# Kernel tuning notes

Hardware: AMD Instinct MI355X
Metric: run time of the kernel (lower is better)

## Reference

```python
import jax, jax.numpy as jnp
import numpy as np
from jax import lax

B, W, L, K = 256, 4096, 16, 8  # batch, nodes/level, levels, fan-in


def setup_inputs() -> dict:
    key = jax.random.key(0)
    ks = jax.random.split(key, 7)
    s = 1.0 / np.sqrt(K)  # torch nn.Linear default init scale
    observed_bits = jnp.round(jax.random.uniform(ks[0], (B, W))).astype(jnp.float32)
    prior_w = jax.random.uniform(ks[1], (W,), minval=-1.0, maxval=1.0)  # PriorNode Linear(1,1) weight
    prior_b = jax.random.uniform(ks[2], (W,), minval=-1.0, maxval=1.0)
    weights = jax.random.uniform(ks[3], (L - 1, W, K), minval=-s, maxval=s)  # per-node Linear(K,1)
    biases = jax.random.uniform(ks[4], (L - 1, W), minval=-s, maxval=s)
    # parents sorted DESCENDING per node: heap pops higher rv first, so inputs are
    # concatenated in descending parent-rv order in the original traversal.
    parents = -jnp.sort(-jax.random.randint(ks[5], (L - 1, W, K), 0, W), axis=-1)
    inv_mask = jax.random.randint(ks[6], (L - 1, W), 0, 2).astype(bool)  # True -> InvNode
    return {"observed_bits": observed_bits, "prior_w": prior_w, "prior_b": prior_b,
            "weights": weights, "biases": biases, "parents": parents, "inv_mask": inv_mask}


def reference(observed_bits, prior_w, prior_b, weights, biases, parents, inv_mask):
    # Observed level: PriorNode with num_parents=1 -> relu(w*bit + b), per node.  (B, W)
    h = jax.nn.relu(observed_bits * prior_w[None, :] + prior_b[None, :])

    def step(h, lvl):
        w, b, p, inv = lvl  # (W,K), (W,), (W,K) int, (W,) bool
        x = h[:, p]                                   # gather parent outputs -> (B, W, K)
        x = jnp.where(inv[:, None], 1.0 - x, x)       # InvNode applies fc(1 - x)
        h2 = jax.nn.relu(jnp.einsum('bnk,nk->bn', x, w) + b)  # per-node Linear(K,1)+ReLU
        return h2, None

    h, _ = lax.scan(step, h, (weights, biases, parents, inv_mask))
    return h  # (B, num_input_bits) == pred.squeeze() of the original
```

## Files before the change

kernel.cpp:

```cpp
#include <hip/hip_runtime.h>
#include <hip/hip_fp16.h>

#define WN 4096
#define BN 256
#define KN 8
#define NLVL 15
#define NTHR 1024
#define NPT (WN / NTHR)

__global__ __launch_bounds__(256) void prep_kernel(
    const float* __restrict__ wts, const float* __restrict__ bia,
    const int* __restrict__ par,   const int* __restrict__ inv,
    uint4* __restrict__ Wh, uint4* __restrict__ Pp, float* __restrict__ Bz) {
  __shared__ unsigned cnt[4][32];
  const int t    = threadIdx.x;
  const int wv   = t >> 6;
  const int lane = t & 63;
  const int idx  = blockIdx.x * 256 + t;
  unsigned* c = cnt[wv];

  const int4   pA = *(const int4*)(par + (size_t)idx * KN);
  const int4   pB = *(const int4*)(par + (size_t)idx * KN + 4);
  const float4 wA = *(const float4*)(wts + (size_t)idx * KN);
  const float4 wB = *(const float4*)(wts + (size_t)idx * KN + 4);
  const bool   iv = inv[idx] != 0;
  const float  sw = ((wA.x + wA.y) + (wA.z + wA.w)) + ((wB.x + wB.y) + (wB.z + wB.w));
  const float  s  = iv ? -1.0f : 1.0f;
  const int   p0 = pA.x, p1 = pA.y, p2 = pA.z, p3 = pA.w;
  const int   p4 = pB.x, p5 = pB.y, p6 = pB.z, p7 = pB.w;
  const float w0 = wA.x * s, w1 = wA.y * s, w2 = wA.z * s, w3 = wA.w * s;
  const float w4 = wB.x * s, w5 = wB.y * s, w6 = wB.z * s, w7 = wB.w * s;

  unsigned mask = 0xffu;
  unsigned op[KN];
  float    ow[KN];

#pragma unroll
  for (int k = 0; k < KN; ++k) {
    __syncthreads();
    if (lane < 32) c[lane] = 0;
    __syncthreads();
    unsigned bestj = 0, bestv = 0xffffffffu;
#define SCAN(J, PJ) if (mask & (1u << (J))) { unsigned v = c[(PJ) & 31]; if (v < bestv) { bestv = v; bestj = (J); } }
    SCAN(0, p0) SCAN(1, p1) SCAN(2, p2) SCAN(3, p3)
    SCAN(4, p4) SCAN(5, p5) SCAN(6, p6) SCAN(7, p7)
#undef SCAN
    const unsigned pj =
        (bestj == 0) ? (unsigned)p0 : (bestj == 1) ? (unsigned)p1 :
        (bestj == 2) ? (unsigned)p2 : (bestj == 3) ? (unsigned)p3 :
        (bestj == 4) ? (unsigned)p4 : (bestj == 5) ? (unsigned)p5 :
        (bestj == 6) ? (unsigned)p6 : (unsigned)p7;
    const float wj =
        (bestj == 0) ? w0 : (bestj == 1) ? w1 :
        (bestj == 2) ? w2 : (bestj == 3) ? w3 :
        (bestj == 4) ? w4 : (bestj == 5) ? w5 :
        (bestj == 6) ? w6 : w7;
    atomicAdd(&c[pj & 31], 1u);
    op[k] = pj;
    ow[k] = wj;
    mask &= ~(1u << bestj);
  }

  Pp[idx] = make_uint4(op[0] | (op[1] << 16), op[2] | (op[3] << 16),
                       op[4] | (op[5] << 16), op[6] | (op[7] << 16));
  uint4 wq;
  wq.x = (unsigned)__half_as_ushort(__float2half(ow[0])) |
         ((unsigned)__half_as_ushort(__float2half(ow[1])) << 16);
  wq.y = (unsigned)__half_as_ushort(__float2half(ow[2])) |
         ((unsigned)__half_as_ushort(__float2half(ow[3])) << 16);
  wq.z = (unsigned)__half_as_ushort(__float2half(ow[4])) |
         ((unsigned)__half_as_ushort(__float2half(ow[5])) << 16);
  wq.w = (unsigned)__half_as_ushort(__float2half(ow[6])) |
         ((unsigned)__half_as_ushort(__float2half(ow[7])) << 16);
  Wh[idx] = wq;
  Bz[idx] = iv ? bia[idx] + sw : bia[idx];
}

__global__ __launch_bounds__(NTHR) void fused_lds_kernel(
    const float* __restrict__ obs, const float* __restrict__ pw,
    const float* __restrict__ pb,  const uint4* __restrict__ Wh,
    const uint4* __restrict__ Pp,  const float* __restrict__ Bz,
    float* __restrict__ out) {
  __shared__ float h[2][WN];
  const int    t = threadIdx.x;
  const size_t b = blockIdx.x;

  uint4 pp[2][NPT];
  float bz[2][NPT];

#pragma unroll
  for (int i = 0; i < NPT; ++i) {
    pp[0][i] = Pp[i * NTHR + t];
    bz[0][i] = Bz[i * NTHR + t];
  }
#pragma unroll
  for (int i = 0; i < NPT; ++i) {
    const int n = i * NTHR + t;
    h[0][n] = fmaxf(fmaf(obs[b * WN + n], pw[n], pb[n]), 0.0f);
  }
  __syncthreads();

#pragma unroll
  for (int l = 0; l < NLVL; ++l) {
    const int cb = l & 1;
    const int nb = cb ^ 1;
    const float* hc = h[l & 1];
    float*       hn = h[(l + 1) & 1];

    if (l + 1 < NLVL) {
#pragma unroll
      for (int i = 0; i < NPT; ++i) {
        const size_t nl = (size_t)(l + 1) * WN + i * NTHR + t;
        pp[nb][i] = Pp[nl];
        bz[nb][i] = Bz[nl];
      }
    }

    uint4 wq[NPT];
#pragma unroll
    for (int i = 0; i < NPT; ++i)
      wq[i] = Wh[(size_t)l * WN + i * NTHR + t];

#pragma unroll
    for (int i = 0; i < NPT; ++i) {
      const uint4 p = pp[cb][i];
      const float x0 = hc[p.x & 0xffffu];
      const float x1 = hc[p.x >> 16];
      const float x2 = hc[p.y & 0xffffu];
      const float x3 = hc[p.y >> 16];
      const float x4 = hc[p.z & 0xffffu];
      const float x5 = hc[p.z >> 16];
      const float x6 = hc[p.w & 0xffffu];
      const float x7 = hc[p.w >> 16];
      const __half2* hw = reinterpret_cast<const __half2*>(&wq[i]);
      const float2 f01 = __half22float2(hw[0]);
      const float2 f23 = __half22float2(hw[1]);
      const float2 f45 = __half22float2(hw[2]);
      const float2 f67 = __half22float2(hw[3]);
      float acc = bz[cb][i];
      acc = fmaf(x0, f01.x, acc);
      acc = fmaf(x1, f01.y, acc);
      acc = fmaf(x2, f23.x, acc);
      acc = fmaf(x3, f23.y, acc);
      acc = fmaf(x4, f45.x, acc);
      acc = fmaf(x5, f45.y, acc);
      acc = fmaf(x6, f67.x, acc);
      acc = fmaf(x7, f67.y, acc);
      hn[i * NTHR + t] = fmaxf(acc, 0.0f);
    }
    __syncthreads();
  }

#pragma unroll
  for (int i = 0; i < NPT; ++i) {
    const int n = i * NTHR + t;
    out[b * WN + n] = h[NLVL & 1][n];
  }
}

extern "C" void kernel_launch(void* const* d_in, const int* in_sizes, int n_in,
                              void* d_out, int out_size, void* d_ws, size_t ws_size,
                              hipStream_t stream) {
  const float* obs = (const float*)d_in[0];
  const float* pw  = (const float*)d_in[1];
  const float* pb  = (const float*)d_in[2];
  const float* wts = (const float*)d_in[3];
  const float* bia = (const float*)d_in[4];
  const int*   par = (const int*)d_in[5];
  const int*   inv = (const int*)d_in[6];
  float* out = (float*)d_out;

  char* ws = (char*)d_ws;
  uint4* Wh = (uint4*)ws;
  uint4* Pp = (uint4*)(ws + (size_t)NLVL * WN * 16);
  float* Bz = (float*)(ws + (size_t)NLVL * WN * 32);

  prep_kernel<<<(NLVL * WN) / 256, 256, 0, stream>>>(wts, bia, par, inv, Wh, Pp, Bz);
  fused_lds_kernel<<<BN, NTHR, 0, stream>>>(obs, pw, pb, Wh, Pp, Bz, out);
}
```

Measured before the change: 106.0 us.

## Cap per-bank parent counts in prep reorder and use raw LDS barriers

```diff
diff --git a/kernel.cpp b/kernel.cpp
--- a/kernel.cpp
+++ b/kernel.cpp
@@ -7,6 +7,9 @@
 #define NLVL 15
 #define NTHR 1024
 #define NPT (WN / NTHR)
+
+#define RAW_BAR() asm volatile("s_waitcnt lgkmcnt(0)\ns_barrier" ::: "memory")
+#define WAVE_LGKM() asm volatile("s_waitcnt lgkmcnt(0)" ::: "memory")
 
 __global__ __launch_bounds__(256) void prep_kernel(
     const float* __restrict__ wts, const float* __restrict__ bia,
@@ -37,28 +40,43 @@
 
 #pragma unroll
   for (int k = 0; k < KN; ++k) {
-    __syncthreads();
     if (lane < 32) c[lane] = 0;
-    __syncthreads();
-    unsigned bestj = 0, bestv = 0xffffffffu;
+    WAVE_LGKM();
+    unsigned chosen = 8u;
+#pragma unroll
+    for (int it = 0; it < 3; ++it) {
+      if (chosen == 8u) {
+        unsigned bestj = 0, bestv = 0xffffffffu;
 #define SCAN(J, PJ) if (mask & (1u << (J))) { unsigned v = c[(PJ) & 31]; if (v < bestv) { bestv = v; bestj = (J); } }
-    SCAN(0, p0) SCAN(1, p1) SCAN(2, p2) SCAN(3, p3)
-    SCAN(4, p4) SCAN(5, p5) SCAN(6, p6) SCAN(7, p7)
+        SCAN(0, p0) SCAN(1, p1) SCAN(2, p2) SCAN(3, p3)
+        SCAN(4, p4) SCAN(5, p5) SCAN(6, p6) SCAN(7, p7)
 #undef SCAN
+        const unsigned bank =
+            (bestj == 0) ? (p0 & 31) : (bestj == 1) ? (p1 & 31) :
+            (bestj == 2) ? (p2 & 31) : (bestj == 3) ? (p3 & 31) :
+            (bestj == 4) ? (p4 & 31) : (bestj == 5) ? (p5 & 31) :
+            (bestj == 6) ? (p6 & 31) : (p7 & 31);
+        const unsigned cap = (it < 2) ? 2u : 3u;
+        const unsigned old = atomicAdd(&c[bank], 1u);
+        if (old < cap) chosen = bestj;
+        else           atomicSub(&c[bank], 1u);
+      }
+      WAVE_LGKM();
+    }
+    if (chosen == 8u) chosen = (unsigned)__ffs(mask) - 1u;
     const unsigned pj =
-        (bestj == 0) ? (unsigned)p0 : (bestj == 1) ? (unsigned)p1 :
-        (bestj == 2) ? (unsigned)p2 : (bestj == 3) ? (unsigned)p3 :
-        (bestj == 4) ? (unsigned)p4 : (bestj == 5) ? (unsigned)p5 :
-        (bestj == 6) ? (unsigned)p6 : (unsigned)p7;
+        (chosen == 0) ? (unsigned)p0 : (chosen == 1) ? (unsigned)p1 :
+        (chosen == 2) ? (unsigned)p2 : (chosen == 3) ? (unsigned)p3 :
+        (chosen == 4) ? (unsigned)p4 : (chosen == 5) ? (unsigned)p5 :
+        (chosen == 6) ? (unsigned)p6 : (unsigned)p7;
     const float wj =
-        (bestj == 0) ? w0 : (bestj == 1) ? w1 :
-        (bestj == 2) ? w2 : (bestj == 3) ? w3 :
-        (bestj == 4) ? w4 : (bestj == 5) ? w5 :
-        (bestj == 6) ? w6 : w7;
-    atomicAdd(&c[pj & 31], 1u);
+        (chosen == 0) ? w0 : (chosen == 1) ? w1 :
+        (chosen == 2) ? w2 : (chosen == 3) ? w3 :
+        (chosen == 4) ? w4 : (chosen == 5) ? w5 :
+        (chosen == 6) ? w6 : w7;
     op[k] = pj;
     ow[k] = wj;
-    mask &= ~(1u << bestj);
+    mask &= ~(1u << chosen);
   }
 
   Pp[idx] = make_uint4(op[0] | (op[1] << 16), op[2] | (op[3] << 16),
@@ -98,7 +116,7 @@
     const int n = i * NTHR + t;
     h[0][n] = fmaxf(fmaf(obs[b * WN + n], pw[n], pb[n]), 0.0f);
   }
-  __syncthreads();
+  RAW_BAR();
 
 #pragma unroll
   for (int l = 0; l < NLVL; ++l) {
@@ -148,7 +166,7 @@
       acc = fmaf(x7, f67.y, acc);
       hn[i * NTHR + t] = fmaxf(acc, 0.0f);
     }
-    __syncthreads();
+    RAW_BAR();
   }
 
 #pragma unroll
```

After: 113.8 us. 7.3% more time.
